# Kernel optimization log

Hardware: AMD Instinct MI355X
Metric: run time of the kernel (lower is better)

The kernel has to match this reference:

```python
import jax, jax.numpy as jnp
import numpy as np


def setup_inputs() -> dict:
    key = jax.random.key(0)
    k1, k2 = jax.random.split(key)
    B, C, H, W = 4, 128, 192, 192
    x = jax.random.normal(k1, (B, C, H, W), dtype=jnp.float32)
    y = jax.random.normal(k2, (B, C, H, W), dtype=jnp.float32)
    return {"x": x, "y": y, "kernel_size": 9, "stride": 1}


def reference(x, y, kernel_size, stride):
    # FlowNet-style correlation volume: for each displacement offset in a
    # kernel_size x kernel_size window (spacing = stride), compute the
    # channel-mean dot product between x and the shifted y.
    # Output: [B, kernel_size**2, H, W]
    B, C, H, W = x.shape
    d = kernel_size // 2          # displacement radius in offset units
    pad = d * stride              # spatial padding so all shifts are valid
    y_pad = jnp.pad(y, ((0, 0), (0, 0), (pad, pad), (pad, pad)))
    inv_c = jnp.float32(1.0 / C)
    outs = []
    # small fixed loop over kernel_size**2 offsets (81 for k=9); each
    # iteration is a fused elementwise-multiply + channel reduction.
    for i in range(kernel_size):
        for j in range(kernel_size):
            ys = jax.lax.dynamic_slice(
                y_pad, (0, 0, i * stride, j * stride), (B, C, H, W))
            outs.append(jnp.sum(x * ys, axis=1) * inv_c)  # [B, H, W]
    return jnp.stack(outs, axis=1)  # [B, k*k, H, W]
```

## Files before the change

### kernel.cpp

```cpp
#include <hip/hip_runtime.h>
#include <hip/hip_bf16.h>

typedef short bf16x8 __attribute__((ext_vector_type(8)));
typedef float f32x4  __attribute__((ext_vector_type(4)));
typedef unsigned short us4 __attribute__((ext_vector_type(4)));

#define NT 512

__device__ __forceinline__ unsigned short f2bf(float f) {
    __hip_bfloat16 h = __float2bfloat16(f);
    return reinterpret_cast<const unsigned short&>(h);
}

__global__ __launch_bounds__(NT, 4)
void corr_k(const float* __restrict__ x, const float* __restrict__ y,
            float* __restrict__ out)
{
    constexpr int H = 192, W = 192;
    const int plane = H * W;
    const int pl4   = plane * 4;

    __shared__ __align__(16) unsigned short ylds[12 * 32 * 32];
    __shared__ float olds[8 * 192];

    const int bid  = blockIdx.x;
    const int task = (bid & 7) * 288 + (bid >> 3);
    const int ht   = task % 48;
    const int r1   = task / 48;
    const int wt   = r1 % 12;
    const int b    = r1 / 12;
    const int h0 = ht * 4, w0 = wt * 16;

    const int tid  = threadIdx.x;
    const int wid  = tid >> 6;
    const int lane = tid & 63;
    const int lm = lane & 15, lg = lane >> 4;
    const int sel  = (lm >> 1) & 3;
    const int r    = wid >> 1;
    const int half = wid & 1;
    const int dy0  = half ? 4 : 0;

    const unsigned boff = (unsigned)b * 128u * (unsigned)pl4;

    unsigned yoff[5]; int lidx[5]; float okf[5];
#pragma unroll
    for (int k = 0; k < 5; ++k) {
        int t = tid + k * NT;
        if (t >= 2304) t = tid;
        const int w = t % 24, q = t / 24;
        const int cg = q & 7, row = q >> 3;
        const int hg = h0 - 4 + row, wg = w0 - 4 + w;
        const int hc = min(max(hg, 0), H - 1);
        const int wc = min(max(wg, 0), W - 1);
        okf[k] = ((hg >= 0) & (hg < H) & (wg >= 0) & (wg < W)) ? 1.0f : 0.0f;
        yoff[k] = boff + (unsigned)(cg * 4) * (unsigned)pl4 + (unsigned)(hc * W + wc) * 4u;
        lidx[k] = row * 1024 + w * 32 + (((cg >> 1) ^ ((w >> 1) & 3)) << 3) + (cg & 1) * 4;
    }
    const unsigned xoff = boff + (unsigned)(lg * 8) * (unsigned)pl4
                        + (unsigned)((h0 + r) * W + (w0 + lm)) * 4u;

    const char* __restrict__ yB = (const char*)y;
    const char* __restrict__ xB = (const char*)x;

    float ypf[5][4]; float xpf[8];
    bf16x8 a;
    f32x4 acc[5][2];
#pragma unroll
    for (int i = 0; i < 5; ++i) {
        acc[i][0] = (f32x4){0.f, 0.f, 0.f, 0.f};
        acc[i][1] = (f32x4){0.f, 0.f, 0.f, 0.f};
    }

    auto ISSUE = [&](int ck) {
        const unsigned co = (unsigned)ck * 32u * (unsigned)pl4;
#pragma unroll
        for (int k = 0; k < 4; ++k) {
            const char* p = yB + (yoff[k] + co);
#pragma unroll
            for (int j = 0; j < 4; ++j) ypf[k][j] = *(const float*)(p + j * pl4);
        }
        if (tid < 256) {
            const char* p = yB + (yoff[4] + co);
#pragma unroll
            for (int j = 0; j < 4; ++j) ypf[4][j] = *(const float*)(p + j * pl4);
        }
        const char* px = xB + (xoff + co);
#pragma unroll
        for (int j = 0; j < 8; ++j) xpf[j] = *(const float*)(px + j * pl4);
    };

    auto CVTWRITE = [&]() {
#pragma unroll
        for (int k = 0; k < 4; ++k) {
            us4 pk = { f2bf(ypf[k][0] * okf[k]), f2bf(ypf[k][1] * okf[k]),
                       f2bf(ypf[k][2] * okf[k]), f2bf(ypf[k][3] * okf[k]) };
            *reinterpret_cast<us4*>(&ylds[lidx[k]]) = pk;
        }
        if (tid < 256) {
            us4 pk = { f2bf(ypf[4][0] * okf[4]), f2bf(ypf[4][1] * okf[4]),
                       f2bf(ypf[4][2] * okf[4]), f2bf(ypf[4][3] * okf[4]) };
            *reinterpret_cast<us4*>(&ylds[lidx[4]]) = pk;
        }
#pragma unroll
        for (int j = 0; j < 8; ++j) a[j] = (short)f2bf(xpf[j]);
    };

    auto COMPUTE = [&]() {
        const int rbase = (r + dy0) * 1024 + lm * 32 + ((lg ^ sel) << 3);
#pragma unroll
        for (int i = 0; i < 4; ++i) {
            const bf16x8 b0 = *reinterpret_cast<const bf16x8*>(&ylds[rbase + i * 1024]);
            const bf16x8 b1 = *reinterpret_cast<const bf16x8*>(&ylds[rbase + i * 1024 + 512]);
            acc[i][0] = __builtin_amdgcn_mfma_f32_16x16x32_bf16(a, b0, acc[i][0], 0, 0, 0);
            acc[i][1] = __builtin_amdgcn_mfma_f32_16x16x32_bf16(a, b1, acc[i][1], 0, 0, 0);
        }
        if (half) {
            const bf16x8 b0 = *reinterpret_cast<const bf16x8*>(&ylds[rbase + 4096]);
            const bf16x8 b1 = *reinterpret_cast<const bf16x8*>(&ylds[rbase + 4096 + 512]);
            acc[4][0] = __builtin_amdgcn_mfma_f32_16x16x32_bf16(a, b0, acc[4][0], 0, 0, 0);
            acc[4][1] = __builtin_amdgcn_mfma_f32_16x16x32_bf16(a, b1, acc[4][1], 0, 0, 0);
        }
    };

    ISSUE(0);
    CVTWRITE();
    __syncthreads();
    ISSUE(1);
    COMPUTE();
#pragma unroll
    for (int ck = 1; ck < 4; ++ck) {
        __syncthreads();
        CVTWRITE();
        __syncthreads();
        if (ck < 3) ISSUE(ck + 1);
        COMPUTE();
    }

    const float invc = 1.0f / 128.0f;
    float* my = olds + wid * 192;
    int woff[8];
#pragma unroll
    for (int q = 0; q < 8; ++q) {
        const int nt = q >> 2, j = q & 3;
        const int m = lg * 4 + j;
        const int dxx = lm + nt * 16 - m;
        woff[q] = (dxx >= 0 && dxx <= 8) ? dxx * 17 + m : 160 + (lane & 31);
    }
    int ridx[3]; unsigned soff[3];
#pragma unroll
    for (int p = 0; p < 3; ++p) {
        const int idx = p * 64 + lane;
        const int dxr = idx >> 4, mr = idx & 15;
        ridx[p] = dxr * 17 + mr;
        soff[p] = (unsigned)(dxr * plane + mr) * 4u;
    }
    char* ob = (char*)out + ((size_t)b * 81 * plane + (size_t)(h0 + r) * W + w0) * 4;

#pragma unroll
    for (int i = 0; i < 5; ++i) {
        if (i < 4 || half) {
            const int dy = dy0 + i;
#pragma unroll
            for (int q = 0; q < 8; ++q)
                my[woff[q]] = acc[i][q >> 2][q & 3] * invc;
            const unsigned dyoff = (unsigned)(dy * 9 * plane) * 4u;
#pragma unroll
            for (int p = 0; p < 3; ++p) {
                if (p < 2 || lane < 16) {
                    const float v = my[ridx[p]];
                    *(float*)(ob + (size_t)(dyoff + soff[p])) = v;
                }
            }
        }
    }
}

extern "C" void kernel_launch(void* const* d_in, const int* in_sizes, int n_in,
                              void* d_out, int out_size, void* d_ws, size_t ws_size,
                              hipStream_t stream)
{
    const float* x = (const float*)d_in[0];
    const float* y = (const float*)d_in[1];
    float* out = (float*)d_out;
    corr_k<<<2304, NT, 0, stream>>>(x, y, out);
}
```

Before: 236.6 us.

## Double tile height, stage x and y via LDS with vectorized loads, 64-channel chunks

Each block now covers an 8x16 output tile with 1024 threads, which halves the grid and the redundant loading of the y halo. Both x and y are staged through a 140KB LDS buffer using 16-byte vector global loads, bf16 conversion and 16-byte swizzled LDS writes. The channel loop is cut to two 64-channel chunks with double buffering. The large LDS footprint allows only one block per CU and the launch_bounds is unchanged, so the lower occupancy and longer per-stage latency may offset the gain in reuse.

Result: no change. 232.2 us (-1.9%).

```diff
diff --git a/kernel.cpp b/kernel.cpp
--- a/kernel.cpp
+++ b/kernel.cpp
@@ -3,9 +3,9 @@
 
 typedef short bf16x8 __attribute__((ext_vector_type(8)));
 typedef float f32x4  __attribute__((ext_vector_type(4)));
-typedef unsigned short us4 __attribute__((ext_vector_type(4)));
+typedef unsigned short us8 __attribute__((ext_vector_type(8)));
 
-#define NT 512
+#define NT 1024
 
 __device__ __forceinline__ unsigned short f2bf(float f) {
     __hip_bfloat16 h = __float2bfloat16(f);
@@ -17,53 +17,57 @@
             float* __restrict__ out)
 {
     constexpr int H = 192, W = 192;
-    const int plane = H * W;
-    const int pl4   = plane * 4;
+    constexpr int plane = H * W;
+    constexpr int pl4   = plane * 4;
+    constexpr int CHB   = 64 * pl4;
 
-    __shared__ __align__(16) unsigned short ylds[12 * 32 * 32];
-    __shared__ float olds[8 * 192];
+    __shared__ __align__(16) char smem[143360];
 
     const int bid  = blockIdx.x;
-    const int task = (bid & 7) * 288 + (bid >> 3);
-    const int ht   = task % 48;
-    const int r1   = task / 48;
+    const int task = (bid & 7) * 144 + (bid >> 3);
+    const int ht   = task % 24;
+    const int r1   = task / 24;
     const int wt   = r1 % 12;
     const int b    = r1 / 12;
-    const int h0 = ht * 4, w0 = wt * 16;
+    const int h0 = ht * 8, w0 = wt * 16;
 
     const int tid  = threadIdx.x;
     const int wid  = tid >> 6;
     const int lane = tid & 63;
     const int lm = lane & 15, lg = lane >> 4;
-    const int sel  = (lm >> 1) & 3;
-    const int r    = wid >> 1;
-    const int half = wid & 1;
-    const int dy0  = half ? 4 : 0;
+    const int r = wid >> 1, half = wid & 1, dy0 = half ? 4 : 0;
 
     const unsigned boff = (unsigned)b * 128u * (unsigned)pl4;
 
-    unsigned yoff[5]; int lidx[5]; float okf[5];
+    const char* gptr; char* lptr; int dstride; float okf;
+    int lwo[4];
+    if (tid < 768) {
+        const int cg = tid & 7, w4 = (tid >> 3) % 6, row = tid / 48;
+        const int hg = h0 - 4 + row, wg = w0 - 4 + w4 * 4;
+        okf = ((hg >= 0) & (hg < H) & (wg >= 0) & (wg <= W - 4)) ? 1.f : 0.f;
+        const int hc = min(max(hg, 0), H - 1);
+        const int wc = min(max(wg, 0), W - 4);
+        gptr = (const char*)y + (boff + (unsigned)(cg * 8) * pl4
+                                 + (unsigned)(hc * W + wc) * 4u);
+        lptr = smem + row * 3072 + w4 * 512;
+        dstride = 49152;
 #pragma unroll
-    for (int k = 0; k < 5; ++k) {
-        int t = tid + k * NT;
-        if (t >= 2304) t = tid;
-        const int w = t % 24, q = t / 24;
-        const int cg = q & 7, row = q >> 3;
-        const int hg = h0 - 4 + row, wg = w0 - 4 + w;
-        const int hc = min(max(hg, 0), H - 1);
-        const int wc = min(max(wg, 0), W - 1);
-        okf[k] = ((hg >= 0) & (hg < H) & (wg >= 0) & (wg < W)) ? 1.0f : 0.0f;
-        yoff[k] = boff + (unsigned)(cg * 4) * (unsigned)pl4 + (unsigned)(hc * W + wc) * 4u;
-        lidx[k] = row * 1024 + w * 32 + (((cg >> 1) ^ ((w >> 1) & 3)) << 3) + (cg & 1) * 4;
+        for (int w = 0; w < 4; ++w)
+            lwo[w] = w * 128 + ((cg ^ ((w4 * 4 + w) & 7)) << 4);
+    } else {
+        const int t = tid - 768;
+        const int cg = t & 7, w4 = (t >> 3) & 3, row = t >> 5;
+        okf = 1.f;
+        gptr = (const char*)x + (boff + (unsigned)(cg * 8) * pl4
+                                 + (unsigned)((h0 + row) * W + w0 + w4 * 4) * 4u);
+        lptr = smem + 98304 + row * 2048 + w4 * 512;
+        dstride = 16384;
+#pragma unroll
+        for (int w = 0; w < 4; ++w)
+            lwo[w] = w * 128 + ((cg ^ ((w4 * 4 + w) & 7)) << 4);
     }
-    const unsigned xoff = boff + (unsigned)(lg * 8) * (unsigned)pl4
-                        + (unsigned)((h0 + r) * W + (w0 + lm)) * 4u;
 
-    const char* __restrict__ yB = (const char*)y;
-    const char* __restrict__ xB = (const char*)x;
-
-    float ypf[5][4]; float xpf[8];
-    bf16x8 a;
+    f32x4 pf[8];
     f32x4 acc[5][2];
 #pragma unroll
     for (int i = 0; i < 5; ++i) {
@@ -71,73 +75,57 @@
         acc[i][1] = (f32x4){0.f, 0.f, 0.f, 0.f};
     }
 
-    auto ISSUE = [&](int ck) {
-        const unsigned co = (unsigned)ck * 32u * (unsigned)pl4;
+    const int so0 = ((lg ^ (lm & 7)) << 4);
+    const int so1 = so0 ^ 64;
+
+    auto STAGE = [&](int ck) {
 #pragma unroll
-        for (int k = 0; k < 4; ++k) {
-            const char* p = yB + (yoff[k] + co);
+        for (int j = 0; j < 8; ++j)
+            pf[j] = *reinterpret_cast<const f32x4*>(gptr + ck * CHB + j * pl4);
+    };
+    auto CVTW = [&](int ck) {
+        char* d = lptr + (ck & 1) * dstride;
 #pragma unroll
-            for (int j = 0; j < 4; ++j) ypf[k][j] = *(const float*)(p + j * pl4);
+        for (int w = 0; w < 4; ++w) {
+            us8 v = { f2bf(pf[0][w] * okf), f2bf(pf[1][w] * okf),
+                      f2bf(pf[2][w] * okf), f2bf(pf[3][w] * okf),
+                      f2bf(pf[4][w] * okf), f2bf(pf[5][w] * okf),
+                      f2bf(pf[6][w] * okf), f2bf(pf[7][w] * okf) };
+            *reinterpret_cast<us8*>(d + lwo[w]) = v;
         }
-        if (tid < 256) {
-            const char* p = yB + (yoff[4] + co);
+    };
+    auto COMPUTE = [&](int buf) {
+        const char* xb = smem + 98304 + buf * 16384 + r * 2048 + lm * 128;
+        const bf16x8 a0 = *reinterpret_cast<const bf16x8*>(xb + so0);
+        const bf16x8 a1 = *reinterpret_cast<const bf16x8*>(xb + so1);
+        const char* yb0 = smem + buf * 49152 + (r + dy0) * 3072 + lm * 128;
 #pragma unroll
-            for (int j = 0; j < 4; ++j) ypf[4][j] = *(const float*)(p + j * pl4);
-        }
-        const char* px = xB + (xoff + co);
-#pragma unroll
-        for (int j = 0; j < 8; ++j) xpf[j] = *(const float*)(px + j * pl4);
-    };
-
-    auto CVTWRITE = [&]() {
-#pragma unroll
-        for (int k = 0; k < 4; ++k) {
-            us4 pk = { f2bf(ypf[k][0] * okf[k]), f2bf(ypf[k][1] * okf[k]),
-                       f2bf(ypf[k][2] * okf[k]), f2bf(ypf[k][3] * okf[k]) };
-            *reinterpret_cast<us4*>(&ylds[lidx[k]]) = pk;
-        }
-        if (tid < 256) {
-            us4 pk = { f2bf(ypf[4][0] * okf[4]), f2bf(ypf[4][1] * okf[4]),
-                       f2bf(ypf[4][2] * okf[4]), f2bf(ypf[4][3] * okf[4]) };
-            *reinterpret_cast<us4*>(&ylds[lidx[4]]) = pk;
-        }
-#pragma unroll
-        for (int j = 0; j < 8; ++j) a[j] = (short)f2bf(xpf[j]);
-    };
-
-    auto COMPUTE = [&]() {
-        const int rbase = (r + dy0) * 1024 + lm * 32 + ((lg ^ sel) << 3);
-#pragma unroll
-        for (int i = 0; i < 4; ++i) {
-            const bf16x8 b0 = *reinterpret_cast<const bf16x8*>(&ylds[rbase + i * 1024]);
-            const bf16x8 b1 = *reinterpret_cast<const bf16x8*>(&ylds[rbase + i * 1024 + 512]);
-            acc[i][0] = __builtin_amdgcn_mfma_f32_16x16x32_bf16(a, b0, acc[i][0], 0, 0, 0);
-            acc[i][1] = __builtin_amdgcn_mfma_f32_16x16x32_bf16(a, b1, acc[i][1], 0, 0, 0);
-        }
-        if (half) {
-            const bf16x8 b0 = *reinterpret_cast<const bf16x8*>(&ylds[rbase + 4096]);
-            const bf16x8 b1 = *reinterpret_cast<const bf16x8*>(&ylds[rbase + 4096 + 512]);
-            acc[4][0] = __builtin_amdgcn_mfma_f32_16x16x32_bf16(a, b0, acc[4][0], 0, 0, 0);
-            acc[4][1] = __builtin_amdgcn_mfma_f32_16x16x32_bf16(a, b1, acc[4][1], 0, 0, 0);
+        for (int i = 0; i < 5; ++i) {
+            if (i < 4 || half) {
+                const char* yb = yb0 + i * 3072;
+                const bf16x8 b00 = *reinterpret_cast<const bf16x8*>(yb + so0);
+                const bf16x8 b01 = *reinterpret_cast<const bf16x8*>(yb + 2048 + so0);
+                const bf16x8 b10 = *reinterpret_cast<const bf16x8*>(yb + so1);
+                const bf16x8 b11 = *reinterpret_cast<const bf16x8*>(yb + 2048 + so1);
+                acc[i][0] = __builtin_amdgcn_mfma_f32_16x16x32_bf16(a0, b00, acc[i][0], 0, 0, 0);
+                acc[i][1] = __builtin_amdgcn_mfma_f32_16x16x32_bf16(a0, b01, acc[i][1], 0, 0, 0);
+                acc[i][0] = __builtin_amdgcn_mfma_f32_16x16x32_bf16(a1, b10, acc[i][0], 0, 0, 0);
+                acc[i][1] = __builtin_amdgcn_mfma_f32_16x16x32_bf16(a1, b11, acc[i][1], 0, 0, 0);
+            }
         }
     };
 
-    ISSUE(0);
-    CVTWRITE();
+    STAGE(0);
+    CVTW(0);
+    STAGE(1);
     __syncthreads();
-    ISSUE(1);
-    COMPUTE();
-#pragma unroll
-    for (int ck = 1; ck < 4; ++ck) {
-        __syncthreads();
-        CVTWRITE();
-        __syncthreads();
-        if (ck < 3) ISSUE(ck + 1);
-        COMPUTE();
-    }
+    COMPUTE(0);
+    CVTW(1);
+    __syncthreads();
+    COMPUTE(1);
 
     const float invc = 1.0f / 128.0f;
-    float* my = olds + wid * 192;
+    float* my = (float*)(smem + 131072) + wid * 192;
     int woff[8];
 #pragma unroll
     for (int q = 0; q < 8; ++q) {
@@ -146,16 +134,15 @@
         const int dxx = lm + nt * 16 - m;
         woff[q] = (dxx >= 0 && dxx <= 8) ? dxx * 17 + m : 160 + (lane & 31);
     }
-    int ridx[3]; unsigned soff[3];
+    int ridx[3], soff[3];
 #pragma unroll
     for (int p = 0; p < 3; ++p) {
         const int idx = p * 64 + lane;
         const int dxr = idx >> 4, mr = idx & 15;
         ridx[p] = dxr * 17 + mr;
-        soff[p] = (unsigned)(dxr * plane + mr) * 4u;
+        soff[p] = dxr * plane + mr;
     }
-    char* ob = (char*)out + ((size_t)b * 81 * plane + (size_t)(h0 + r) * W + w0) * 4;
-
+    float* ob = out + (size_t)b * 81 * plane + (size_t)(h0 + r) * W + w0;
 #pragma unroll
     for (int i = 0; i < 5; ++i) {
         if (i < 4 || half) {
@@ -163,14 +150,11 @@
 #pragma unroll
             for (int q = 0; q < 8; ++q)
                 my[woff[q]] = acc[i][q >> 2][q & 3] * invc;
-            const unsigned dyoff = (unsigned)(dy * 9 * plane) * 4u;
+            const int dyoff = dy * 9 * plane;
 #pragma unroll
-            for (int p = 0; p < 3; ++p) {
-                if (p < 2 || lane < 16) {
-                    const float v = my[ridx[p]];
-                    *(float*)(ob + (size_t)(dyoff + soff[p])) = v;
-                }
-            }
+            for (int p = 0; p < 3; ++p)
+                if (p < 2 || lane < 16)
+                    ob[dyoff + soff[p]] = my[ridx[p]];
         }
     }
 }
@@ -182,5 +166,5 @@
     const float* x = (const float*)d_in[0];
     const float* y = (const float*)d_in[1];
     float* out = (float*)d_out;
-    corr_k<<<2304, NT, 0, stream>>>(x, y, out);
+    corr_k<<<1152, NT, 0, stream>>>(x, y, out);
 }
```
